# Optimization experiments

Hardware: AMD Instinct MI355X
Metric: run time of the kernel (lower is better)

The kernel has to match this reference:

```python
import jax, jax.numpy as jnp
import numpy as np

QP = 127.0          # 2**(8-1)-1, signed symmetric int8
MIN_RANGE = 1e-6


def _ste_round(x):
    # round_pass: forward round, straight-through gradient
    return x + jax.lax.stop_gradient(jnp.round(x) - x)


def _quant_per_tensor(x):
    # symmetric per-tensor: scale = max|x| / Qp (grad flows through max as in source)
    scale = jnp.maximum(jnp.max(jnp.abs(x)), MIN_RANGE) / QP
    return _ste_round(x / scale), scale


def _qlinear(x2d, w, b):
    # faithful to _quantize_global (prefix_token_num=None path):
    #   out = (x_q @ w_q.T + bias) * (s_w * s_x)
    xq, sx = _quant_per_tensor(x2d)
    wq, sw = _quant_per_tensor(w)
    out = jnp.matmul(xq, wq.T) + b[None, :]
    return out * (sw * sx)


def setup_inputs() -> dict:
    key = jax.random.key(0)
    k = jax.random.split(key, 5)
    B, N, D, H = 8, 1024, 1024, 4096
    return {
        "x": jax.random.normal(k[0], (B, N, D), dtype=jnp.float32),
        "w1": jax.random.normal(k[1], (H, D), dtype=jnp.float32) * 0.02,
        "b1": jax.random.normal(k[2], (H,), dtype=jnp.float32) * 0.02,
        "w2": jax.random.normal(k[3], (D, H), dtype=jnp.float32) * 0.02,
        "b2": jax.random.normal(k[4], (D,), dtype=jnp.float32) * 0.02,
    }


def reference(x, w1, b1, w2, b2):
    B, N, D = x.shape
    h = _qlinear(x.reshape(-1, D), w1, b1)          # [B*N, H]
    h = jax.nn.gelu(h, approximate=False)            # exact GELU (nn.GELU default)
    o = _qlinear(h, w2, b2)                          # [B*N, D]
    return o.reshape(B, N, -1)
```

## Files before the change

### kernel.cpp

```cpp
#include <hip/hip_runtime.h>
#include <hip/hip_fp16.h>
#include <cstdint>
#include <cmath>

#define QP    127.0f
#define MINR  1e-6f

#define MTOK 8192
#define DDIM 1024
#define HDIM 4096

typedef __attribute__((ext_vector_type(4))) int int32x4;
typedef __attribute__((ext_vector_type(8))) short short8;

__device__ __forceinline__ void gload16(const void* g, void* l) {
    __builtin_amdgcn_global_load_lds(
        (const __attribute__((address_space(1))) void*)g,
        (__attribute__((address_space(3))) void*)l, 16, 0, 0);
}

__global__ void zero_scales_kernel(float* g) {
    if (threadIdx.x < 4) g[threadIdx.x] = 0.0f;
}

__device__ __forceinline__ float wave_block_max(float m) {
    #pragma unroll
    for (int off = 32; off; off >>= 1) m = fmaxf(m, __shfl_down(m, off));
    __shared__ float sm[4];
    int lane = threadIdx.x & 63, w = threadIdx.x >> 6;
    if (lane == 0) sm[w] = m;
    __syncthreads();
    float bm = 0.0f;
    if (threadIdx.x == 0) bm = fmaxf(fmaxf(sm[0], sm[1]), fmaxf(sm[2], sm[3]));
    return bm;
}

__device__ __forceinline__ void absmax_range(const float4* in4, int n4, int bid, int nb,
                                             float* gout) {
    int tid = bid * blockDim.x + threadIdx.x;
    int stride = nb * blockDim.x;
    float m = 0.0f;
    for (int i = tid; i < n4; i += stride) {
        float4 v = in4[i];
        m = fmaxf(m, fmaxf(fmaxf(fabsf(v.x), fabsf(v.y)), fmaxf(fabsf(v.z), fabsf(v.w))));
    }
    float bm = wave_block_max(m);
    if (threadIdx.x == 0) atomicMax((int*)gout, __float_as_int(bm));
}

__global__ void absmax3_kernel(const float* __restrict__ x, const float* __restrict__ w1,
                               const float* __restrict__ w2, float* __restrict__ gmax) {
    int b = blockIdx.x;
    if (b < 1024)      absmax_range((const float4*)x,  MTOK * DDIM / 4, b,        1024, gmax + 0);
    else if (b < 1536) absmax_range((const float4*)w1, HDIM * DDIM / 4, b - 1024,  512, gmax + 1);
    else               absmax_range((const float4*)w2, DDIM * HDIM / 4, b - 1536,  512, gmax + 3);
}

__device__ __forceinline__ void quant_range(const float4* in4, int* out4, int n4,
                                            int bid, int nb, const float* gm) {
    const float s = fmaxf(*gm, MINR) / QP;
    int tid = bid * blockDim.x + threadIdx.x;
    int stride = nb * blockDim.x;
    for (int i = tid; i < n4; i += stride) {
        float4 v = in4[i];
        int q0 = ((int)rintf(v.x / s)) & 255;
        int q1 = ((int)rintf(v.y / s)) & 255;
        int q2 = ((int)rintf(v.z / s)) & 255;
        int q3 = ((int)rintf(v.w / s)) & 255;
        out4[i] = q0 | (q1 << 8) | (q2 << 16) | (q3 << 24);
    }
}

__global__ void quant3_kernel(const float* __restrict__ x, const float* __restrict__ w1,
                              const float* __restrict__ w2, int8_t* __restrict__ xq,
                              int8_t* __restrict__ w1q, int8_t* __restrict__ w2q,
                              const float* __restrict__ gmax) {
    int b = blockIdx.x;
    if (b < 2048)      quant_range((const float4*)x,  (int*)xq,  MTOK * DDIM / 4, b,        2048, gmax + 0);
    else if (b < 3072) quant_range((const float4*)w1, (int*)w1q, HDIM * DDIM / 4, b - 2048, 1024, gmax + 1);
    else               quant_range((const float4*)w2, (int*)w2q, DDIM * HDIM / 4, b - 3072, 1024, gmax + 3);
}

__global__ void quant_h_kernel(const __half* __restrict__ h, int8_t* __restrict__ hq,
                               const float* __restrict__ gm) {
    const float s = fmaxf(*gm, MINR) / QP;
    const short8* in8 = (const short8*)h;
    int2* out8 = (int2*)hq;
    const int n8 = MTOK * HDIM / 8;
    int tid = blockIdx.x * blockDim.x + threadIdx.x;
    int stride = gridDim.x * blockDim.x;
    for (int i = tid; i < n8; i += stride) {
        short8 v = in8[i];
        int q[8];
        #pragma unroll
        for (int j = 0; j < 8; ++j) {
            __half_raw r; r.x = (unsigned short)v[j];
            float f = __half2float(__half(r));
            q[j] = ((int)rintf(f / s)) & 255;
        }
        int2 o;
        o.x = q[0] | (q[1] << 8) | (q[2] << 16) | (q[3] << 24);
        o.y = q[4] | (q[5] << 8) | (q[6] << 16) | (q[7] << 24);
        out8[i] = o;
    }
}

template<int KD, int ND, bool GELU_EPI, typename OUTT>
__global__ __launch_bounds__(256, 2)
void gemm_i8_kernel(const int8_t* __restrict__ A, const int8_t* __restrict__ B,
                    const float* __restrict__ bias,
                    const float* __restrict__ gmA, const float* __restrict__ gmB,
                    OUTT* __restrict__ out, float* __restrict__ omax) {
    constexpr int NBC = ND / 128;
    __shared__ int8_t lA[128 * 128];
    __shared__ int8_t lB[128 * 128];
    const int t = threadIdx.x;
    const int lane = t & 63;
    const int w = t >> 6;
    const int wm = (w >> 1) * 64;
    const int wn = (w & 1) * 64;
    const int lr = lane & 15;
    const int lg = lane >> 4;

    const int chunk = gridDim.x >> 3;
    const int logical = (blockIdx.x & 7) * chunk + (blockIdx.x >> 3);
    const int bc = logical % NBC;
    const int br = logical / NBC;

    const int8_t* Ab = A + (size_t)br * 128 * KD;
    const int8_t* Bb = B + (size_t)bc * 128 * KD;

    int32x4 acc[4][4] = {};

    for (int kt = 0; kt < KD / 128; ++kt) {
        #pragma unroll
        for (int i = 0; i < 4; ++i) {
            int c = t + i * 256;
            int r = c >> 3;
            int sl = c & 7;
            int sc = ((sl ^ (r & 7)) << 4);
            gload16(Ab + (size_t)r * KD + kt * 128 + sc, &lA[c * 16]);
            gload16(Bb + (size_t)r * KD + kt * 128 + sc, &lB[c * 16]);
        }
        __syncthreads();

        #pragma unroll
        for (int kk = 0; kk < 2; ++kk) {
            int32x4 af[4], bf[4];
            #pragma unroll
            for (int m = 0; m < 4; ++m) {
                int r = wm + m * 16 + lr;
                int g = kk * 4 + lg;
                af[m] = *(const int32x4*)&lA[r * 128 + ((g ^ (r & 7)) << 4)];
            }
            #pragma unroll
            for (int n = 0; n < 4; ++n) {
                int r = wn + n * 16 + lr;
                int g = kk * 4 + lg;
                bf[n] = *(const int32x4*)&lB[r * 128 + ((g ^ (r & 7)) << 4)];
            }
            #pragma unroll
            for (int m = 0; m < 4; ++m)
                #pragma unroll
                for (int n = 0; n < 4; ++n)
                    acc[m][n] = __builtin_amdgcn_mfma_i32_16x16x64_i8(af[m], bf[n], acc[m][n], 0, 0, 0);
        }
        __syncthreads();
    }

    const float sA = fmaxf(*gmA, MINR) / QP;
    const float sB = fmaxf(*gmB, MINR) / QP;
    const float s = sB * sA;
    float lmax = 0.0f;
    #pragma unroll
    for (int m = 0; m < 4; ++m) {
        #pragma unroll
        for (int n = 0; n < 4; ++n) {
            #pragma unroll
            for (int r = 0; r < 4; ++r) {
                int row = br * 128 + wm + m * 16 + lg * 4 + r;
                int col = bc * 128 + wn + n * 16 + lr;
                float f = (float)acc[m][n][r] + bias[col];
                f *= s;
                if (GELU_EPI) {
                    float gg = f * (erff(f / 1.41421356237309504880f) + 1.0f) * 0.5f;
                    out[(size_t)row * ND + col] = (OUTT)gg;
                    lmax = fmaxf(lmax, fabsf(gg));
                } else {
                    out[(size_t)row * ND + col] = (OUTT)f;
                }
            }
        }
    }
    if (GELU_EPI) {
        #pragma unroll
        for (int off = 32; off; off >>= 1) lmax = fmaxf(lmax, __shfl_down(lmax, off));
        __shared__ float red[4];
        if (lane == 0) red[w] = lmax;
        __syncthreads();
        if (t == 0) {
            float bm = fmaxf(fmaxf(red[0], red[1]), fmaxf(red[2], red[3]));
            atomicMax((int*)omax, __float_as_int(bm));
        }
    }
}

extern "C" void kernel_launch(void* const* d_in, const int* in_sizes, int n_in,
                              void* d_out, int out_size, void* d_ws, size_t ws_size,
                              hipStream_t stream) {
    const float* x  = (const float*)d_in[0];
    const float* w1 = (const float*)d_in[1];
    const float* b1 = (const float*)d_in[2];
    const float* w2 = (const float*)d_in[3];
    const float* b2 = (const float*)d_in[4];
    float* out = (float*)d_out;

    uint8_t* ws = (uint8_t*)d_ws;
    float*  gmax = (float*)ws;
    int8_t* xq   = (int8_t*)(ws + 256);
    int8_t* w1q  = xq  + (size_t)MTOK * DDIM;
    int8_t* w2q  = w1q + (size_t)HDIM * DDIM;
    int8_t* hq   = w2q + (size_t)DDIM * HDIM;
    __half* h    = (__half*)(hq + (size_t)MTOK * HDIM);

    zero_scales_kernel<<<1, 64, 0, stream>>>(gmax);

    absmax3_kernel<<<2048, 256, 0, stream>>>(x, w1, w2, gmax);
    quant3_kernel<<<4096, 256, 0, stream>>>(x, w1, w2, xq, w1q, w2q, gmax);

    gemm_i8_kernel<DDIM, HDIM, true, __half>
        <<<2048, 256, 0, stream>>>(xq, w1q, b1, gmax + 0, gmax + 1, h, gmax + 2);

    quant_h_kernel<<<2048, 256, 0, stream>>>(h, hq, gmax + 2);

    gemm_i8_kernel<HDIM, DDIM, false, float>
        <<<512, 256, 0, stream>>>(hq, w2q, b2, gmax + 2, gmax + 3, out, nullptr);
}
```

Baseline: 193.0 us.

## Enlarge int8 GEMM tiles to 256xBN with 512-thread blocks

Both int8 GEMMs now use 256-row block tiles: 256x256 for the first GEMM and 256x128 for the second. Blocks grow to 8 waves, and each wave computes a 128xBN/4 sub-tile, so more MFMA work is done per LDS fragment load and per global byte. The grouped block-index swizzle is replaced by a plain 2D grid. The cost is many more accumulator registers per thread (up to 128 int32 in GEMM1), which may cause spills or lower occupancy. The second GEMM gets only 256 blocks, fewer than a good fill of the device.

New measurement: 218.8 us. 13.3% more time.

```diff
diff --git a/kernel.cpp b/kernel.cpp
--- a/kernel.cpp
+++ b/kernel.cpp
@@ -105,64 +105,66 @@
     }
 }
 
-template<int KD, int ND, bool GELU_EPI, typename OUTT>
-__global__ __launch_bounds__(256, 2)
+template<int KD, int ND, int BN, bool GELU_EPI, typename OUTT>
+__global__ __launch_bounds__(512, 2)
 void gemm_i8_kernel(const int8_t* __restrict__ A, const int8_t* __restrict__ B,
                     const float* __restrict__ bias,
                     const float* __restrict__ gmA, const float* __restrict__ gmB,
                     OUTT* __restrict__ out, float* __restrict__ omax) {
-    constexpr int NBC = ND / 128;
-    __shared__ int8_t lA[128 * 128];
-    __shared__ int8_t lB[128 * 128];
+    constexpr int BM = 256;
+    constexpr int NF = (BN / 4) / 16;
+    __shared__ int8_t lA[BM * 128];
+    __shared__ int8_t lB[BN * 128];
     const int t = threadIdx.x;
     const int lane = t & 63;
     const int w = t >> 6;
-    const int wm = (w >> 1) * 64;
-    const int wn = (w & 1) * 64;
+    const int wm = (w >> 2) * 128;
+    const int wn = (w & 3) * (BN / 4);
     const int lr = lane & 15;
     const int lg = lane >> 4;
-
-    const int chunk = gridDim.x >> 3;
-    const int logical = (blockIdx.x & 7) * chunk + (blockIdx.x >> 3);
-    const int bc = logical % NBC;
-    const int br = logical / NBC;
-
-    const int8_t* Ab = A + (size_t)br * 128 * KD;
-    const int8_t* Bb = B + (size_t)bc * 128 * KD;
-
-    int32x4 acc[4][4] = {};
+    const int br = blockIdx.y, bc = blockIdx.x;
+
+    const int8_t* Ab = A + (size_t)br * BM * KD;
+    const int8_t* Bb = B + (size_t)bc * BN * KD;
+
+    int32x4 acc[8][NF] = {};
 
     for (int kt = 0; kt < KD / 128; ++kt) {
         #pragma unroll
         for (int i = 0; i < 4; ++i) {
-            int c = t + i * 256;
+            int c = t + i * 512;
             int r = c >> 3;
             int sl = c & 7;
-            int sc = ((sl ^ (r & 7)) << 4);
-            gload16(Ab + (size_t)r * KD + kt * 128 + sc, &lA[c * 16]);
-            gload16(Bb + (size_t)r * KD + kt * 128 + sc, &lB[c * 16]);
+            gload16(Ab + (size_t)r * KD + kt * 128 + ((sl ^ (r & 7)) << 4), &lA[c * 16]);
+        }
+        #pragma unroll
+        for (int i = 0; i < BN / 64; ++i) {
+            int c = t + i * 512;
+            int r = c >> 3;
+            int sl = c & 7;
+            gload16(Bb + (size_t)r * KD + kt * 128 + ((sl ^ (r & 7)) << 4), &lB[c * 16]);
         }
         __syncthreads();
 
         #pragma unroll
         for (int kk = 0; kk < 2; ++kk) {
-            int32x4 af[4], bf[4];
-            #pragma unroll
-            for (int m = 0; m < 4; ++m) {
+            int32x4 af[8], bf[NF];
+            #pragma unroll
+            for (int m = 0; m < 8; ++m) {
                 int r = wm + m * 16 + lr;
                 int g = kk * 4 + lg;
                 af[m] = *(const int32x4*)&lA[r * 128 + ((g ^ (r & 7)) << 4)];
             }
             #pragma unroll
-            for (int n = 0; n < 4; ++n) {
+            for (int n = 0; n < NF; ++n) {
                 int r = wn + n * 16 + lr;
                 int g = kk * 4 + lg;
                 bf[n] = *(const int32x4*)&lB[r * 128 + ((g ^ (r & 7)) << 4)];
             }
             #pragma unroll
-            for (int m = 0; m < 4; ++m)
+            for (int m = 0; m < 8; ++m)
                 #pragma unroll
-                for (int n = 0; n < 4; ++n)
+                for (int n = 0; n < NF; ++n)
                     acc[m][n] = __builtin_amdgcn_mfma_i32_16x16x64_i8(af[m], bf[n], acc[m][n], 0, 0, 0);
         }
         __syncthreads();
@@ -173,13 +175,13 @@
     const float s = sB * sA;
     float lmax = 0.0f;
     #pragma unroll
-    for (int m = 0; m < 4; ++m) {
-        #pragma unroll
-        for (int n = 0; n < 4; ++n) {
+    for (int m = 0; m < 8; ++m) {
+        #pragma unroll
+        for (int n = 0; n < NF; ++n) {
             #pragma unroll
             for (int r = 0; r < 4; ++r) {
-                int row = br * 128 + wm + m * 16 + lg * 4 + r;
-                int col = bc * 128 + wn + n * 16 + lr;
+                int row = br * BM + wm + m * 16 + lg * 4 + r;
+                int col = bc * BN + wn + n * 16 + lr;
                 float f = (float)acc[m][n][r] + bias[col];
                 f *= s;
                 if (GELU_EPI) {
@@ -195,11 +197,13 @@
     if (GELU_EPI) {
         #pragma unroll
         for (int off = 32; off; off >>= 1) lmax = fmaxf(lmax, __shfl_down(lmax, off));
-        __shared__ float red[4];
+        __shared__ float red[8];
         if (lane == 0) red[w] = lmax;
         __syncthreads();
         if (t == 0) {
-            float bm = fmaxf(fmaxf(red[0], red[1]), fmaxf(red[2], red[3]));
+            float bm = red[0];
+            #pragma unroll
+            for (int i = 1; i < 8; ++i) bm = fmaxf(bm, red[i]);
             atomicMax((int*)omax, __float_as_int(bm));
         }
     }
@@ -228,11 +232,11 @@
     absmax3_kernel<<<2048, 256, 0, stream>>>(x, w1, w2, gmax);
     quant3_kernel<<<4096, 256, 0, stream>>>(x, w1, w2, xq, w1q, w2q, gmax);
 
-    gemm_i8_kernel<DDIM, HDIM, true, __half>
-        <<<2048, 256, 0, stream>>>(xq, w1q, b1, gmax + 0, gmax + 1, h, gmax + 2);
+    gemm_i8_kernel<DDIM, HDIM, 256, true, __half>
+        <<<dim3(16, 32), 512, 0, stream>>>(xq, w1q, b1, gmax + 0, gmax + 1, h, gmax + 2);
 
     quant_h_kernel<<<2048, 256, 0, stream>>>(h, hq, gmax + 2);
 
-    gemm_i8_kernel<HDIM, DDIM, false, float>
-        <<<512, 256, 0, stream>>>(hq, w2q, b2, gmax + 2, gmax + 3, out, nullptr);
-}
+    gemm_i8_kernel<HDIM, DDIM, 128, false, float>
+        <<<dim3(8, 32), 512, 0, stream>>>(hq, w2q, b2, gmax + 2, gmax + 3, out, nullptr);
+}
```

## Double-buffer int8 GEMM K-loop with 64-wide tiles and new LDS swizzle

Applied to the files above, without the earlier changes.

Reworks the int8 MFMA GEMM main loop to use two 128x64 LDS stages per operand, issuing the global-to-LDS loads for the next K slice before computing on the current one, with a single wait and barrier per step. The goal is to hide global load latency behind MFMA work instead of leaving a load, barrier, compute, barrier sequence. It also changes the XOR swizzle to suit 64-byte rows and drops the XCD-aware block remapping in favour of a plain 2D grid, which may reduce L2 locality across chiplets. LDS usage per block stays the same.

Result: slower. 213.2 us (+10.5%).

```diff
diff --git a/kernel.cpp b/kernel.cpp
--- a/kernel.cpp
+++ b/kernel.cpp
@@ -111,9 +111,9 @@
                     const float* __restrict__ bias,
                     const float* __restrict__ gmA, const float* __restrict__ gmB,
                     OUTT* __restrict__ out, float* __restrict__ omax) {
-    constexpr int NBC = ND / 128;
-    __shared__ int8_t lA[128 * 128];
-    __shared__ int8_t lB[128 * 128];
+    constexpr int KT = KD / 64;
+    __shared__ int8_t lA[2 * 128 * 64];
+    __shared__ int8_t lB[2 * 128 * 64];
     const int t = threadIdx.x;
     const int lane = t & 63;
     const int w = t >> 6;
@@ -121,52 +121,56 @@
     const int wn = (w & 1) * 64;
     const int lr = lane & 15;
     const int lg = lane >> 4;
-
-    const int chunk = gridDim.x >> 3;
-    const int logical = (blockIdx.x & 7) * chunk + (blockIdx.x >> 3);
-    const int bc = logical % NBC;
-    const int br = logical / NBC;
+    const int br = blockIdx.y, bc = blockIdx.x;
 
     const int8_t* Ab = A + (size_t)br * 128 * KD;
     const int8_t* Bb = B + (size_t)bc * 128 * KD;
 
+    const int swz = ((lg ^ (lr & 3) ^ ((lr >> 2) & 3)) << 4);
+
     int32x4 acc[4][4] = {};
 
-    for (int kt = 0; kt < KD / 128; ++kt) {
-        #pragma unroll
-        for (int i = 0; i < 4; ++i) {
-            int c = t + i * 256;
-            int r = c >> 3;
-            int sl = c & 7;
-            int sc = ((sl ^ (r & 7)) << 4);
-            gload16(Ab + (size_t)r * KD + kt * 128 + sc, &lA[c * 16]);
-            gload16(Bb + (size_t)r * KD + kt * 128 + sc, &lB[c * 16]);
-        }
-        __syncthreads();
-
-        #pragma unroll
-        for (int kk = 0; kk < 2; ++kk) {
-            int32x4 af[4], bf[4];
-            #pragma unroll
-            for (int m = 0; m < 4; ++m) {
-                int r = wm + m * 16 + lr;
-                int g = kk * 4 + lg;
-                af[m] = *(const int32x4*)&lA[r * 128 + ((g ^ (r & 7)) << 4)];
-            }
-            #pragma unroll
-            for (int n = 0; n < 4; ++n) {
-                int r = wn + n * 16 + lr;
-                int g = kk * 4 + lg;
-                bf[n] = *(const int32x4*)&lB[r * 128 + ((g ^ (r & 7)) << 4)];
-            }
-            #pragma unroll
-            for (int m = 0; m < 4; ++m)
-                #pragma unroll
-                for (int n = 0; n < 4; ++n)
-                    acc[m][n] = __builtin_amdgcn_mfma_i32_16x16x64_i8(af[m], bf[n], acc[m][n], 0, 0, 0);
-        }
-        __syncthreads();
-    }
+#define STAGE(S, kt_) do {                                                        \
+        _Pragma("unroll") for (int i_ = 0; i_ < 2; ++i_) {                        \
+            int c_ = t + i_ * 256;                                    \
+            int r_ = c_ >> 2;                                     \
+            int sl_ = c_ & 3;                                  \
+            int sc_ = ((sl_ ^ (r_ & 3) ^ ((r_ >> 2) & 3)) << 4);                  \
+            gload16(Ab + (size_t)r_ * KD + (kt_) * 64 + sc_, &lA[(S) * 8192 + c_ * 16]); \
+            gload16(Bb + (size_t)r_ * KD + (kt_) * 64 + sc_, &lB[(S) * 8192 + c_ * 16]); \
+        } } while (0)
+
+#define COMPUTE(S) do {                                                           \
+        int32x4 af[4], bf[4];                                                     \
+        _Pragma("unroll") for (int m = 0; m < 4; ++m)                             \
+            af[m] = *(const int32x4*)&lA[(S) * 8192 + (wm + m * 16 + lr) * 64 + swz]; \
+        _Pragma("unroll") for (int n = 0; n < 4; ++n)                             \
+            bf[n] = *(const int32x4*)&lB[(S) * 8192 + (wn + n * 16 + lr) * 64 + swz]; \
+        _Pragma("unroll") for (int m = 0; m < 4; ++m)                             \
+            _Pragma("unroll") for (int n = 0; n < 4; ++n)                         \
+                acc[m][n] = __builtin_amdgcn_mfma_i32_16x16x64_i8(af[m], bf[n], acc[m][n], 0, 0, 0); \
+        } while (0)
+
+#define SYNC() do {                                                               \
+        asm volatile("s_waitcnt vmcnt(0) lgkmcnt(0)" ::: "memory");               \
+        __builtin_amdgcn_s_barrier();                                             \
+        asm volatile("" ::: "memory");                                            \
+        } while (0)
+
+    STAGE(0, 0);
+    SYNC();
+
+    for (int kt = 0; kt < KT; kt += 2) {
+        if (kt + 1 < KT) STAGE(1, kt + 1);
+        COMPUTE(0);
+        SYNC();
+        if (kt + 2 < KT) STAGE(0, kt + 2);
+        COMPUTE(1);
+        SYNC();
+    }
+#undef STAGE
+#undef COMPUTE
+#undef SYNC
 
     const float sA = fmaxf(*gmA, MINR) / QP;
     const float sB = fmaxf(*gmB, MINR) / QP;
@@ -229,10 +233,10 @@
     quant3_kernel<<<4096, 256, 0, stream>>>(x, w1, w2, xq, w1q, w2q, gmax);
 
     gemm_i8_kernel<DDIM, HDIM, true, __half>
-        <<<2048, 256, 0, stream>>>(xq, w1q, b1, gmax + 0, gmax + 1, h, gmax + 2);
+        <<<dim3(32, 64), 256, 0, stream>>>(xq, w1q, b1, gmax + 0, gmax + 1, h, gmax + 2);
 
     quant_h_kernel<<<2048, 256, 0, stream>>>(h, hq, gmax + 2);
 
     gemm_i8_kernel<HDIM, DDIM, false, float>
-        <<<512, 256, 0, stream>>>(hq, w2q, b2, gmax + 2, gmax + 3, out, nullptr);
-}
+        <<<dim3(8, 64), 256, 0, stream>>>(hq, w2q, b2, gmax + 2, gmax + 3, out, nullptr);
+}
```

## Replace first GEMM with 256x256-tile 8-wave pipelined int8 MFMA kernel

Applied to the files above, without the earlier changes.

Adds a new GEMM kernel for the first layer using 256x256 block tiles, 512 threads (8 waves), double-buffered LDS filled by direct global-to-LDS loads, and an 8-phase schedule that interleaves loads with MFMA using explicit vmcnt waits, barriers and setprio. It uses swizzled LDS layouts to avoid bank conflicts and keeps the fused bias/scale/GELU/absmax epilogue. The goal is higher MFMA utilisation and better operand reuse in the dominant GEMM, at the cost of heavy register pressure and fragile hand-coded wait counts.

Result: slower. 202.9 us (+5.1%).

```diff
diff --git a/kernel.cpp b/kernel.cpp
--- a/kernel.cpp
+++ b/kernel.cpp
@@ -17,6 +17,18 @@
     __builtin_amdgcn_global_load_lds(
         (const __attribute__((address_space(1))) void*)g,
         (__attribute__((address_space(3))) void*)l, 16, 0, 0);
+}
+
+template<int N> __device__ __forceinline__ void wait_vmcnt() {
+    if constexpr (N == 0) asm volatile("s_waitcnt vmcnt(0)" ::: "memory");
+    else if constexpr (N == 2) asm volatile("s_waitcnt vmcnt(2)" ::: "memory");
+    else if constexpr (N == 3) asm volatile("s_waitcnt vmcnt(3)" ::: "memory");
+    else if constexpr (N == 4) asm volatile("s_waitcnt vmcnt(4)" ::: "memory");
+}
+
+__device__ __forceinline__ void barf() {
+    __builtin_amdgcn_s_barrier();
+    asm volatile("" ::: "memory");
 }
 
 __global__ void zero_scales_kernel(float* g) {
@@ -102,6 +114,127 @@
         o.x = q[0] | (q[1] << 8) | (q[2] << 16) | (q[3] << 24);
         o.y = q[4] | (q[5] << 8) | (q[6] << 16) | (q[7] << 24);
         out8[i] = o;
+    }
+}
+
+__global__ __launch_bounds__(512, 2)
+void gemm8_i8_g1(const int8_t* __restrict__ A, const int8_t* __restrict__ B,
+                 const float* __restrict__ bias,
+                 const float* __restrict__ gmA, const float* __restrict__ gmB,
+                 __half* __restrict__ out, float* __restrict__ omax) {
+    constexpr int KD = DDIM;
+    constexpr int ND = HDIM;
+    constexpr int ITER = (KD / 64) / 2;
+
+    __shared__ int8_t lA[2 * 16384];
+    __shared__ int8_t lB[2 * 16384];
+
+    const int t = threadIdx.x;
+    const int lane = t & 63;
+    const int w = t >> 6;
+    const int wr = w >> 2;
+    const int wc = w & 3;
+    const int lr = lane & 15;
+    const int lg = lane >> 4;
+    const int br = blockIdx.y, bc = blockIdx.x;
+
+    const int8_t* Ab = A + (size_t)br * 256 * KD;
+    const int8_t* Bb = B + (size_t)bc * 256 * KD;
+
+    const int lam  = t >> 3;
+    const int s8p  = (t & 7) ^ (lam & 7);
+    const int arow = (lam << 1) + (s8p >> 2);
+    const int scol = (s8p & 3) << 4;
+    const int ldst = t * 16;
+    const int grA = (arow & 63) + ((arow >> 6) << 7);
+    const int grB = (arow & 31) + ((arow >> 5) << 6);
+
+    const int s8  = (((((lr & 1) << 2) | lg) ^ (lr >> 1)) << 4);
+    const int rbA = (wr * 32 + (lr >> 1)) * 128 + s8;
+    const int rbB = (wc * 16 + (lr >> 1)) * 128 + s8;
+
+    int32x4 acc[8][4] = {};
+
+#define STA(S, MH, kt_) gload16(Ab + (size_t)(grA + (MH) * 64) * KD + (kt_) * 64 + scol, \
+                                &lA[(S) * 16384 + (MH) * 8192 + ldst])
+#define STB(S, NH, kt_) gload16(Bb + (size_t)(grB + (NH) * 32) * KD + (kt_) * 64 + scol, \
+                                &lB[(S) * 16384 + (NH) * 8192 + ldst])
+
+#define PHASE(P, ...) do {                                                            \
+        constexpr int s_ = (P) >> 2, mh_ = ((P) >> 1) & 1, nh_ = (P) & 1;             \
+        int32x4 af[4], bf[2];                                                         \
+        _Pragma("unroll") for (int m = 0; m < 4; ++m)                                 \
+            af[m] = *(const int32x4*)&lA[s_ * 16384 + mh_ * 8192 + rbA + m * 1024];   \
+        _Pragma("unroll") for (int n = 0; n < 2; ++n)                                 \
+            bf[n] = *(const int32x4*)&lB[s_ * 16384 + nh_ * 8192 + rbB + n * 1024];   \
+        __VA_ARGS__;                                                                  \
+        barf();                                                                       \
+        __builtin_amdgcn_s_setprio(1);                                                \
+        _Pragma("unroll") for (int m = 0; m < 4; ++m)                                 \
+            _Pragma("unroll") for (int n = 0; n < 2; ++n)                             \
+                acc[mh_ * 4 + m][nh_ * 2 + n] = __builtin_amdgcn_mfma_i32_16x16x64_i8(\
+                    af[m], bf[n], acc[mh_ * 4 + m][nh_ * 2 + n], 0, 0, 0);            \
+        __builtin_amdgcn_s_setprio(0);                                                \
+    } while (0)
+
+    STA(0, 0, 0); STB(0, 0, 0); STA(0, 1, 0); STB(0, 1, 0);
+    STA(1, 0, 1); STB(1, 0, 1);
+    wait_vmcnt<2>(); barf();
+
+    for (int it = 0; it < ITER; ++it) {
+        const int k1 = 2 * it + 1, k2 = 2 * it + 2, k3 = 2 * it + 3;
+        const bool more = (it + 1 < ITER);
+        PHASE(0, STA(1, 1, k1));            wait_vmcnt<3>(); barf();
+        PHASE(1, STB(1, 1, k1));            barf();
+        PHASE(2, if (more) STA(0, 0, k2));  barf();
+        PHASE(3, if (more) STB(0, 0, k2));
+            if (more) wait_vmcnt<4>(); else wait_vmcnt<2>();
+            barf();
+        PHASE(4, if (more) STA(0, 1, k2));
+            if (more) wait_vmcnt<3>(); else wait_vmcnt<0>();
+            barf();
+        PHASE(5, if (more) STB(0, 1, k2));  barf();
+        PHASE(6, if (more) STA(1, 0, k3));  barf();
+        PHASE(7, if (more) STB(1, 0, k3));
+            if (more) wait_vmcnt<4>();
+            barf();
+    }
+#undef PHASE
+#undef STA
+#undef STB
+
+    const float sA = fmaxf(*gmA, MINR) / QP;
+    const float sB = fmaxf(*gmB, MINR) / QP;
+    const float s = sB * sA;
+    float lmax = 0.0f;
+    const int rowb = br * 256 + wr * 128 + lg * 4;
+    const int colb = bc * 256 + wc * 64 + lr;
+    #pragma unroll
+    for (int m = 0; m < 8; ++m) {
+        #pragma unroll
+        for (int n = 0; n < 4; ++n) {
+            #pragma unroll
+            for (int r = 0; r < 4; ++r) {
+                int row = rowb + m * 16 + r;
+                int col = colb + n * 16;
+                float f = (float)acc[m][n][r] + bias[col];
+                f *= s;
+                float gg = f * (erff(f / 1.41421356237309504880f) + 1.0f) * 0.5f;
+                out[(size_t)row * ND + col] = (__half)gg;
+                lmax = fmaxf(lmax, fabsf(gg));
+            }
+        }
+    }
+    #pragma unroll
+    for (int off = 32; off; off >>= 1) lmax = fmaxf(lmax, __shfl_down(lmax, off));
+    __shared__ float red[8];
+    if (lane == 0) red[w] = lmax;
+    __syncthreads();
+    if (t == 0) {
+        float bm = red[0];
+        #pragma unroll
+        for (int i = 1; i < 8; ++i) bm = fmaxf(bm, red[i]);
+        atomicMax((int*)omax, __float_as_int(bm));
     }
 }
 
@@ -228,8 +361,7 @@
     absmax3_kernel<<<2048, 256, 0, stream>>>(x, w1, w2, gmax);
     quant3_kernel<<<4096, 256, 0, stream>>>(x, w1, w2, xq, w1q, w2q, gmax);
 
-    gemm_i8_kernel<DDIM, HDIM, true, __half>
-        <<<2048, 256, 0, stream>>>(xq, w1q, b1, gmax + 0, gmax + 1, h, gmax + 2);
+    gemm8_i8_g1<<<dim3(16, 32), 512, 0, stream>>>(xq, w1q, b1, gmax + 0, gmax + 1, h, gmax + 2);
 
     quant_h_kernel<<<2048, 256, 0, stream>>>(h, hq, gmax + 2);
 
```
